# Performance work log

Hardware: AMD Instinct MI355X
Metric: run time of the kernel (lower is better)

The kernel has to match this reference:

```python
import jax, jax.numpy as jnp
import numpy as np
import math

EMB = 2048
N_Q = 32
N_KV = 8
HEAD = EMB // N_Q  # 64
N_REP = N_Q // N_KV  # 4
B, T = 2, 2048
ROPE_BASE = 10000.0


def setup_inputs() -> dict:
    key = jax.random.key(0)
    ks = jax.random.split(key, 9)
    s = 0.02
    return {
        "x": jax.random.normal(ks[0], (B, T, EMB), jnp.float32),
        "Wq": jax.random.normal(ks[1], (EMB, EMB), jnp.float32) * s,
        "bq": jax.random.normal(ks[2], (EMB,), jnp.float32) * s,
        "Wk": jax.random.normal(ks[3], (EMB, N_KV * HEAD), jnp.float32) * s,
        "bk": jax.random.normal(ks[4], (N_KV * HEAD,), jnp.float32) * s,
        "Wv": jax.random.normal(ks[5], (EMB, N_KV * HEAD), jnp.float32) * s,
        "bv": jax.random.normal(ks[6], (N_KV * HEAD,), jnp.float32) * s,
        "Wo": jax.random.normal(ks[7], (EMB, EMB), jnp.float32) * s,
        "bo": jax.random.normal(ks[8], (EMB,), jnp.float32) * s,
    }


def _rope_cos_sin(t, dim, dtype):
    inv_freq = 1.0 / (ROPE_BASE ** (jnp.arange(0, dim, 2, dtype=jnp.float32) / dim))
    freqs = jnp.arange(t, dtype=jnp.float32)[:, None] * inv_freq[None, :]  # (T, D/2)
    emb = jnp.concatenate([freqs, freqs], axis=-1)  # (T, D)
    return jnp.cos(emb).astype(dtype), jnp.sin(emb).astype(dtype)


def _rotate_half(x):
    d = x.shape[-1] // 2
    return jnp.concatenate([-x[..., d:], x[..., :d]], axis=-1)


def reference(x, Wq, bq, Wk, bk, Wv, bv, Wo, bo):
    b, t, c = x.shape
    q = (x @ Wq + bq).reshape(b, t, N_Q, HEAD)
    k = (x @ Wk + bk).reshape(b, t, N_KV, HEAD)
    v = (x @ Wv + bv).reshape(b, t, N_KV, HEAD)

    cos, sin = _rope_cos_sin(t, HEAD, x.dtype)  # (T, HEAD)
    cos = cos[None, :, None, :]
    sin = sin[None, :, None, :]
    q = q * cos + _rotate_half(q) * sin
    k = k * cos + _rotate_half(k) * sin

    # (B, H, T, D)
    q = q.transpose(0, 2, 1, 3)
    k = k.transpose(0, 2, 1, 3)
    v = v.transpose(0, 2, 1, 3)

    # repeat_kv: expand kv heads to match query heads
    k = jnp.repeat(k, N_REP, axis=1)
    v = jnp.repeat(v, N_REP, axis=1)

    scale = 1.0 / math.sqrt(HEAD)
    att = jnp.einsum("bhqd,bhkd->bhqk", q, k) * scale
    causal = jnp.tril(jnp.ones((t, t), dtype=bool))
    att = jnp.where(causal[None, None], att, jnp.finfo(att.dtype).min)
    att = jax.nn.softmax(att, axis=-1)

    y = jnp.einsum("bhqk,bhkd->bhqd", att, v)
    y = y.transpose(0, 2, 1, 3).reshape(b, t, c)
    return y @ Wo + bo
```

## Files before the change

kernel.cpp:

```cpp
#include <hip/hip_runtime.h>
#include <hip/hip_bf16.h>
#include <cstdint>
#include <cstddef>

typedef __attribute__((ext_vector_type(4))) float f32x4;
typedef __attribute__((ext_vector_type(8))) short bf16x8;

#define B_    2
#define T_    2048
#define EMB_  2048
#define NQ_   32
#define NKV_  8
#define HEAD_ 64
#define NTOT_ 3072
#define M_    (B_ * T_)
#define QBLK_ 128

__device__ __forceinline__ unsigned short f2bf(float f) {
  union { float f; unsigned int u; } v; v.f = f;
  unsigned int r = v.u + 0x7fffu + ((v.u >> 16) & 1u);
  return (unsigned short)(r >> 16);
}

__device__ __forceinline__ unsigned int pk_bf16(float lo, float hi) {
  __hip_bfloat162 h = __float22bfloat162_rn(make_float2(lo, hi));
  union { __hip_bfloat162 h; unsigned int u; } c; c.h = h;
  return c.u;
}

__device__ __forceinline__ void gload_lds16(const void* g, void* l) {
  __builtin_amdgcn_global_load_lds(
      (const __attribute__((address_space(1))) void*)g,
      (__attribute__((address_space(3))) void*)l, 16, 0, 0);
}


__global__ void cvt_bf16_kernel(const float* __restrict__ src,
                                unsigned short* __restrict__ dst, int n4) {
  int i = blockIdx.x * blockDim.x + threadIdx.x;
  if (i >= n4) return;
  float4 v = ((const float4*)src)[i];
  unsigned long long pk =
      (unsigned long long)f2bf(v.x) |
      ((unsigned long long)f2bf(v.y) << 16) |
      ((unsigned long long)f2bf(v.z) << 32) |
      ((unsigned long long)f2bf(v.w) << 48);
  *(unsigned long long*)(dst + (size_t)i * 4) = pk;
}

__global__ void transpose_cvt_kernel(const float* __restrict__ src,
                                     unsigned short* __restrict__ dst,
                                     int R, int C) {
  __shared__ float tile[32][33];
  int c0 = blockIdx.x * 32, r0 = blockIdx.y * 32;
  int tx = threadIdx.x, ty = threadIdx.y;
#pragma unroll
  for (int k = 0; k < 4; ++k)
    tile[ty + 8 * k][tx] = src[(size_t)(r0 + ty + 8 * k) * C + c0 + tx];
  __syncthreads();
#pragma unroll
  for (int k = 0; k < 4; ++k)
    dst[(size_t)(c0 + ty + 8 * k) * R + r0 + tx] = f2bf(tile[tx][ty + 8 * k]);
}

__global__ void concat_bias_kernel(const float* __restrict__ bq,
                                   const float* __restrict__ bk,
                                   const float* __restrict__ bv,
                                   float* __restrict__ dst) {
  int i = blockIdx.x * 256 + threadIdx.x;
  if (i < 2048) dst[i] = bq[i];
  else if (i < 2560) dst[i] = bk[i - 2048];
  else if (i < 3072) dst[i] = bv[i - 2560];
}

#define L2_10000 13.2877123795494f

__global__ void rope_q_kernel(const float* __restrict__ qkv,
                              unsigned short* __restrict__ Qh) {
  int idx = blockIdx.x * 256 + threadIdx.x;
  int i  = idx & 31;
  int h  = (idx >> 5) & 31;
  int bt = idx >> 10;
  int t  = bt & (T_ - 1);
  int b  = bt >> 11;
  float invf = exp2f(-(float)i * (L2_10000 / 32.f));
  float ang = (float)t * invf;
  float s, c; sincosf(ang, &s, &c);
  const float* row = qkv + (size_t)bt * NTOT_ + h * 64;
  float x1 = row[i], x2 = row[i + 32];
  unsigned short* q = Qh + ((size_t)(b * NQ_ + h) * T_ + t) * HEAD_;
  q[i]      = f2bf((x1 * c - x2 * s) * 0.125f);
  q[i + 32] = f2bf((x2 * c + x1 * s) * 0.125f);
}

__global__ void rope_k_kernel(const float* __restrict__ qkv,
                              unsigned short* __restrict__ Kh) {
  int idx = blockIdx.x * 256 + threadIdx.x;
  int i  = idx & 31;
  int kh = (idx >> 5) & 7;
  int bt = idx >> 8;
  int t  = bt & (T_ - 1);
  int b  = bt >> 11;
  float invf = exp2f(-(float)i * (L2_10000 / 32.f));
  float ang = (float)t * invf;
  float s, c; sincosf(ang, &s, &c);
  const float* row = qkv + (size_t)bt * NTOT_ + 2048 + kh * 64;
  float x1 = row[i], x2 = row[i + 32];
  unsigned short* kp = Kh + ((size_t)(b * NKV_ + kh) * T_ + t) * HEAD_;
  kp[i]      = f2bf(x1 * c - x2 * s);
  kp[i + 32] = f2bf(x2 * c + x1 * s);
}

__global__ void vt_kernel(const float* __restrict__ qkv,
                          unsigned short* __restrict__ Vt) {
  int idx = blockIdx.x * 256 + threadIdx.x;
  int t  = idx & (T_ - 1);
  int d  = (idx >> 11) & 63;
  int kh = (idx >> 17) & 7;
  int b  = idx >> 20;
  float v = qkv[(size_t)(b * T_ + t) * NTOT_ + 2560 + kh * 64 + d];
  Vt[((size_t)((b * NKV_ + kh) * 64 + d)) * T_ + t] = f2bf(v);
}


__launch_bounds__(256, 2)
__global__ void gemm_bt_bias(const unsigned short* __restrict__ A,
                             const unsigned short* __restrict__ BT,
                             const float* __restrict__ bias,
                             float* __restrict__ C, int N, int K) {
  __shared__ unsigned short Alds[128 * 32];
  __shared__ unsigned short Blds[128 * 32];
  const int tid = threadIdx.x;
  const int wave = tid >> 6, lane = tid & 63;
  const int l16 = lane & 15, lg = lane >> 4;
  const int m0 = blockIdx.x * 128;
  const int n0 = blockIdx.y * 128;
  const int wr = wave >> 1, wc = wave & 1;

  f32x4 zero4 = {0.f, 0.f, 0.f, 0.f};
  f32x4 acc[4][4];
#pragma unroll
  for (int i = 0; i < 4; ++i)
#pragma unroll
    for (int j = 0; j < 4; ++j) acc[i][j] = zero4;

  const int arow = tid >> 2;
  const int kcb  = (tid & 3) * 8;
  const int nk = K >> 5;
  for (int kt = 0; kt < nk; ++kt) {
    const int k0 = kt << 5;
    gload_lds16(A + (size_t)(m0 + arow) * K + k0 + kcb,       (char*)Alds + tid * 16);
    gload_lds16(A + (size_t)(m0 + 64 + arow) * K + k0 + kcb,  (char*)Alds + 4096 + tid * 16);
    gload_lds16(BT + (size_t)(n0 + arow) * K + k0 + kcb,      (char*)Blds + tid * 16);
    gload_lds16(BT + (size_t)(n0 + 64 + arow) * K + k0 + kcb, (char*)Blds + 4096 + tid * 16);
    __syncthreads();
    bf16x8 af[4], bfr[4];
#pragma unroll
    for (int i = 0; i < 4; ++i)
      af[i] = *(const bf16x8*)(Alds + (wr * 64 + i * 16 + l16) * 32 + lg * 8);
#pragma unroll
    for (int j = 0; j < 4; ++j)
      bfr[j] = *(const bf16x8*)(Blds + (wc * 64 + j * 16 + l16) * 32 + lg * 8);
#pragma unroll
    for (int i = 0; i < 4; ++i)
#pragma unroll
      for (int j = 0; j < 4; ++j)
        acc[i][j] = __builtin_amdgcn_mfma_f32_16x16x32_bf16(af[i], bfr[j], acc[i][j], 0, 0, 0);
    __syncthreads();
  }
#pragma unroll
  for (int j = 0; j < 4; ++j) {
    const int col = n0 + wc * 64 + j * 16 + l16;
    const float bv = bias[col];
#pragma unroll
    for (int i = 0; i < 4; ++i) {
      const int rowb = m0 + wr * 64 + i * 16 + lg * 4;
#pragma unroll
      for (int r = 0; r < 4; ++r)
        C[(size_t)(rowb + r) * N + col] = acc[i][j][r] + bv;
    }
  }
}


__launch_bounds__(256, 2)
__global__ void flash_attn_kernel(const unsigned short* __restrict__ Qh,
                                  const unsigned short* __restrict__ Kh,
                                  const unsigned short* __restrict__ Vt,
                                  unsigned short* __restrict__ Y) {
  __shared__ unsigned short Klds[2][64 * 64];
  __shared__ unsigned short Vlds[2][64 * 64];
  __shared__ unsigned short Plds[4][32 * 64];
  const int tid = threadIdx.x;
  const int wave = tid >> 6, lane = tid & 63;
  const int l16 = lane & 15, lg = lane >> 4;
  const int h = blockIdx.y, b = blockIdx.z;
  const int kh = h >> 2;

  const size_t kbase = (size_t)(b * NKV_ + kh) * T_ * HEAD_;
  const size_t vbase = (size_t)(b * NKV_ + kh) * HEAD_ * T_;
  const int srow = tid >> 3;
  const int csrc = (tid & 7) ^ (srow & 7);
  unsigned short* pl = Plds[wave];
  const f32x4 zero4 = {0.f, 0.f, 0.f, 0.f};

#define STAGE(bi, kv0) do {                                                         \
    gload_lds16(Kh + kbase + (size_t)((kv0) + srow) * HEAD_ + csrc * 8,             \
                (char*)Klds[bi] + tid * 16);                                        \
    gload_lds16(Kh + kbase + (size_t)((kv0) + srow + 32) * HEAD_ + csrc * 8,        \
                (char*)Klds[bi] + 4096 + tid * 16);                                 \
    gload_lds16(Vt + vbase + (size_t)srow * T_ + (kv0) + csrc * 8,                  \
                (char*)Vlds[bi] + tid * 16);                                        \
    gload_lds16(Vt + vbase + (size_t)(srow + 32) * T_ + (kv0) + csrc * 8,           \
                (char*)Vlds[bi] + 4096 + tid * 16);                                 \
  } while (0)

  for (int seg = 0; seg < 2; ++seg) {
    const int qt = seg ? (15 - (int)blockIdx.x) : (int)blockIdx.x;
    const int q0 = qt * QBLK_;
    const int nt = (q0 >> 6) + 2;

    bf16x8 aq[2][2];
#pragma unroll
    for (int qh = 0; qh < 2; ++qh) {
      const unsigned short* qp =
          Qh + ((size_t)(b * NQ_ + h) * T_ + q0 + wave * 32 + qh * 16 + l16) * HEAD_;
      aq[qh][0] = *(const bf16x8*)(qp + lg * 8);
      aq[qh][1] = *(const bf16x8*)(qp + 32 + lg * 8);
    }

    f32x4 oacc[2][4];
#pragma unroll
    for (int qh = 0; qh < 2; ++qh)
#pragma unroll
      for (int df = 0; df < 4; ++df) oacc[qh][df] = zero4;
    float mreg[2] = {-1e30f, -1e30f};
    float lp[2] = {0.f, 0.f};

    STAGE(0, 0);

    for (int t = 0; t < nt; ++t) {
      if (t + 1 < nt) {
        STAGE((t + 1) & 1, (t + 1) * 64);
        asm volatile("s_waitcnt vmcnt(4)" ::: "memory");
      } else {
        asm volatile("s_waitcnt vmcnt(0)" ::: "memory");
      }
      __builtin_amdgcn_s_barrier();
      __builtin_amdgcn_sched_barrier(0);

      const unsigned short* Kb = Klds[t & 1];
      const unsigned short* Vb = Vlds[t & 1];
      const int kv0 = t * 64;

      float p[2][4][4];
#pragma unroll
      for (int cf = 0; cf < 4; ++cf) {
        const int krow = cf * 16 + l16;
        const bf16x8 k0 = *(const bf16x8*)(Kb + krow * 64 + ((lg ^ (krow & 7)) << 3));
        const bf16x8 k1 = *(const bf16x8*)(Kb + krow * 64 + (((4 + lg) ^ (krow & 7)) << 3));
#pragma unroll
        for (int qh = 0; qh < 2; ++qh) {
          f32x4 z = zero4;
          z = __builtin_amdgcn_mfma_f32_16x16x32_bf16(k0, aq[qh][0], z, 0, 0, 0);
          z = __builtin_amdgcn_mfma_f32_16x16x32_bf16(k1, aq[qh][1], z, 0, 0, 0);
#pragma unroll
          for (int r = 0; r < 4; ++r) p[qh][cf][r] = z[r];
        }
      }

      if (t >= nt - 2) {
#pragma unroll
        for (int qh = 0; qh < 2; ++qh) {
          const int qg = q0 + wave * 32 + qh * 16 + l16;
#pragma unroll
          for (int cf = 0; cf < 4; ++cf)
#pragma unroll
            for (int r = 0; r < 4; ++r)
              if (kv0 + cf * 16 + lg * 4 + r > qg) p[qh][cf][r] = -1e30f;
        }
      }

#pragma unroll
      for (int qh = 0; qh < 2; ++qh) {
        float pm = p[qh][0][0];
#pragma unroll
        for (int cf = 0; cf < 4; ++cf)
#pragma unroll
          for (int r = 0; r < 4; ++r) pm = fmaxf(pm, p[qh][cf][r]);
        pm = fmaxf(pm, __shfl_xor(pm, 16, 64));
        pm = fmaxf(pm, __shfl_xor(pm, 32, 64));
        const float mnew = fmaxf(mreg[qh], pm);
        const float corr = __expf(mreg[qh] - mnew);
        mreg[qh] = mnew;
        lp[qh] *= corr;
#pragma unroll
        for (int df = 0; df < 4; ++df)
#pragma unroll
          for (int r = 0; r < 4; ++r) oacc[qh][df][r] *= corr;
        float ps = 0.f;
#pragma unroll
        for (int cf = 0; cf < 4; ++cf)
#pragma unroll
          for (int r = 0; r < 4; ++r) {
            const float e = __expf(p[qh][cf][r] - mnew);
            p[qh][cf][r] = e;
            ps += e;
          }
        lp[qh] += ps;
      }

#pragma unroll
      for (int qh = 0; qh < 2; ++qh) {
        const int row = qh * 16 + l16;
#pragma unroll
        for (int cf = 0; cf < 4; ++cf) {
          const unsigned int w0 = pk_bf16(p[qh][cf][0], p[qh][cf][1]);
          const unsigned int w1 = pk_bf16(p[qh][cf][2], p[qh][cf][3]);
          const int u = cf * 2 + (lg >> 1);
          char* ad = (char*)pl + row * 128 + ((u ^ (row & 7)) << 4) + ((lg & 1) << 3);
          *(unsigned long long*)ad =
              (unsigned long long)w0 | ((unsigned long long)w1 << 32);
        }
      }
      bf16x8 pf[2][2];
#pragma unroll
      for (int qh = 0; qh < 2; ++qh) {
        const int row = qh * 16 + l16;
#pragma unroll
        for (int k2 = 0; k2 < 2; ++k2) {
          const int u = k2 * 4 + lg;
          pf[qh][k2] = *(const bf16x8*)((char*)pl + row * 128 + ((u ^ (row & 7)) << 4));
        }
      }

#pragma unroll
      for (int df = 0; df < 4; ++df) {
        const int vrow = df * 16 + l16;
        const bf16x8 v0 = *(const bf16x8*)(Vb + vrow * 64 + ((lg ^ (vrow & 7)) << 3));
        const bf16x8 v1 = *(const bf16x8*)(Vb + vrow * 64 + (((4 + lg) ^ (vrow & 7)) << 3));
#pragma unroll
        for (int qh = 0; qh < 2; ++qh) {
          oacc[qh][df] = __builtin_amdgcn_mfma_f32_16x16x32_bf16(v0, pf[qh][0], oacc[qh][df], 0, 0, 0);
          oacc[qh][df] = __builtin_amdgcn_mfma_f32_16x16x32_bf16(v1, pf[qh][1], oacc[qh][df], 0, 0, 0);
        }
      }

      asm volatile("s_waitcnt lgkmcnt(0)" ::: "memory");
      __builtin_amdgcn_sched_barrier(0);
      __builtin_amdgcn_s_barrier();
    }

#pragma unroll
    for (int qh = 0; qh < 2; ++qh) {
      float lt = lp[qh];
      lt += __shfl_xor(lt, 16, 64);
      lt += __shfl_xor(lt, 32, 64);
      const float inv = 1.f / lt;
      const int tq = q0 + wave * 32 + qh * 16 + l16;
      unsigned short* yp = Y + ((size_t)(b * T_ + tq)) * EMB_ + h * HEAD_;
#pragma unroll
      for (int df = 0; df < 4; ++df) {
        const unsigned int w0 = pk_bf16(oacc[qh][df][0] * inv, oacc[qh][df][1] * inv);
        const unsigned int w1 = pk_bf16(oacc[qh][df][2] * inv, oacc[qh][df][3] * inv);
        *(unsigned long long*)(yp + df * 16 + lg * 4) =
            (unsigned long long)w0 | ((unsigned long long)w1 << 32);
      }
    }
  }
#undef STAGE
}


extern "C" void kernel_launch(void* const* d_in, const int* in_sizes, int n_in,
                              void* d_out, int out_size, void* d_ws, size_t ws_size,
                              hipStream_t stream) {
  const float* x  = (const float*)d_in[0];
  const float* Wq = (const float*)d_in[1];
  const float* bq = (const float*)d_in[2];
  const float* Wk = (const float*)d_in[3];
  const float* bk = (const float*)d_in[4];
  const float* Wv = (const float*)d_in[5];
  const float* bv = (const float*)d_in[6];
  const float* Wo = (const float*)d_in[7];
  const float* bo = (const float*)d_in[8];
  float* out = (float*)d_out;

  char* ws = (char*)d_ws;
  size_t off = 0;
  auto alloc = [&](size_t bytes) {
    void* p = ws + off;
    off += (bytes + 255) & ~(size_t)255;
    return p;
  };
  unsigned short* xb     = (unsigned short*)alloc((size_t)M_ * EMB_ * 2);
  unsigned short* WqkvT  = (unsigned short*)alloc((size_t)NTOT_ * EMB_ * 2);
  unsigned short* WoT    = (unsigned short*)alloc((size_t)EMB_ * EMB_ * 2);
  float*          bcat   = (float*)alloc((size_t)NTOT_ * 4);
  float*          QKVlin = (float*)alloc((size_t)M_ * NTOT_ * 4);
  unsigned short* Qh     = (unsigned short*)alloc((size_t)B_ * NQ_ * T_ * HEAD_ * 2);
  unsigned short* Kh     = (unsigned short*)alloc((size_t)B_ * NKV_ * T_ * HEAD_ * 2);
  unsigned short* Vt     = (unsigned short*)alloc((size_t)B_ * NKV_ * HEAD_ * T_ * 2);
  unsigned short* Yb     = (unsigned short*)alloc((size_t)M_ * EMB_ * 2);

  cvt_bf16_kernel<<<(M_ * EMB_ / 4 + 255) / 256, 256, 0, stream>>>(x, xb, M_ * EMB_ / 4);

  dim3 tb(32, 8);
  transpose_cvt_kernel<<<dim3(EMB_ / 32, EMB_ / 32), tb, 0, stream>>>(Wq, WqkvT, EMB_, EMB_);
  transpose_cvt_kernel<<<dim3(512 / 32, EMB_ / 32), tb, 0, stream>>>(Wk, WqkvT + (size_t)2048 * 2048, EMB_, 512);
  transpose_cvt_kernel<<<dim3(512 / 32, EMB_ / 32), tb, 0, stream>>>(Wv, WqkvT + (size_t)2560 * 2048, EMB_, 512);
  transpose_cvt_kernel<<<dim3(EMB_ / 32, EMB_ / 32), tb, 0, stream>>>(Wo, WoT, EMB_, EMB_);
  concat_bias_kernel<<<(NTOT_ + 255) / 256, 256, 0, stream>>>(bq, bk, bv, bcat);

  gemm_bt_bias<<<dim3(M_ / 128, NTOT_ / 128), 256, 0, stream>>>(xb, WqkvT, bcat, QKVlin, NTOT_, EMB_);

  rope_q_kernel<<<(B_ * T_ * NQ_ * 32) / 256, 256, 0, stream>>>(QKVlin, Qh);
  rope_k_kernel<<<(B_ * T_ * NKV_ * 32) / 256, 256, 0, stream>>>(QKVlin, Kh);
  vt_kernel<<<(B_ * NKV_ * HEAD_ * T_) / 256, 256, 0, stream>>>(QKVlin, Vt);

  flash_attn_kernel<<<dim3(8, NQ_, B_), 256, 0, stream>>>(Qh, Kh, Vt, Yb);

  gemm_bt_bias<<<dim3(M_ / 128, EMB_ / 128), 256, 0, stream>>>(Yb, WoT, bo, out, EMB_, EMB_);

  (void)in_sizes; (void)n_in; (void)out_size; (void)ws_size;
}
```

Measured before the change: 237.7 us.

## Emit bf16 QKV, use exp2 softmax with lazy rescale and MFMA row sums

The QKV projection now writes bf16 instead of fp32, which halves the intermediate traffic read by the rope and V-transpose kernels. The attention softmax folds log2(e) into the Q scale so it can use the raw v_exp_f32 instruction. It skips the running-max rescale unless the max grows by more than 8. Row sums are computed with an extra MFMA against a vector of ones rather than VALU adds and shuffles. This trades some precision (bf16 intermediate, bf16-rounded P in the denominator) for less memory traffic and less VALU work.

New measurement: 231.5 us. 2.6% less time.

```diff
diff --git a/kernel.cpp b/kernel.cpp
--- a/kernel.cpp
+++ b/kernel.cpp
@@ -16,16 +16,28 @@
 #define M_    (B_ * T_)
 #define QBLK_ 128
 
+#define MFMA_ __builtin_amdgcn_mfma_f32_16x16x32_bf16
+
 __device__ __forceinline__ unsigned short f2bf(float f) {
   union { float f; unsigned int u; } v; v.f = f;
   unsigned int r = v.u + 0x7fffu + ((v.u >> 16) & 1u);
   return (unsigned short)(r >> 16);
 }
 
+__device__ __forceinline__ float bf2f(unsigned short u) {
+  union { unsigned int u; float f; } v; v.u = (unsigned int)u << 16; return v.f;
+}
+
 __device__ __forceinline__ unsigned int pk_bf16(float lo, float hi) {
   __hip_bfloat162 h = __float22bfloat162_rn(make_float2(lo, hi));
   union { __hip_bfloat162 h; unsigned int u; } c; c.h = h;
   return c.u;
+}
+
+__device__ __forceinline__ float ex2(float x) {
+  float r;
+  asm("v_exp_f32 %0, %1" : "=v"(r) : "v"(x));
+  return r;
 }
 
 __device__ __forceinline__ void gload_lds16(const void* g, void* l) {
@@ -74,8 +86,9 @@
 }
 
 #define L2_10000 13.2877123795494f
-
-__global__ void rope_q_kernel(const float* __restrict__ qkv,
+#define QSCALE_  0.18033688011112043f
+
+__global__ void rope_q_kernel(const unsigned short* __restrict__ qkv,
                               unsigned short* __restrict__ Qh) {
   int idx = blockIdx.x * 256 + threadIdx.x;
   int i  = idx & 31;
@@ -86,14 +99,14 @@
   float invf = exp2f(-(float)i * (L2_10000 / 32.f));
   float ang = (float)t * invf;
   float s, c; sincosf(ang, &s, &c);
-  const float* row = qkv + (size_t)bt * NTOT_ + h * 64;
-  float x1 = row[i], x2 = row[i + 32];
+  const unsigned short* row = qkv + (size_t)bt * NTOT_ + h * 64;
+  float x1 = bf2f(row[i]), x2 = bf2f(row[i + 32]);
   unsigned short* q = Qh + ((size_t)(b * NQ_ + h) * T_ + t) * HEAD_;
-  q[i]      = f2bf((x1 * c - x2 * s) * 0.125f);
-  q[i + 32] = f2bf((x2 * c + x1 * s) * 0.125f);
-}
-
-__global__ void rope_k_kernel(const float* __restrict__ qkv,
+  q[i]      = f2bf((x1 * c - x2 * s) * QSCALE_);
+  q[i + 32] = f2bf((x2 * c + x1 * s) * QSCALE_);
+}
+
+__global__ void rope_k_kernel(const unsigned short* __restrict__ qkv,
                               unsigned short* __restrict__ Kh) {
   int idx = blockIdx.x * 256 + threadIdx.x;
   int i  = idx & 31;
@@ -104,30 +117,31 @@
   float invf = exp2f(-(float)i * (L2_10000 / 32.f));
   float ang = (float)t * invf;
   float s, c; sincosf(ang, &s, &c);
-  const float* row = qkv + (size_t)bt * NTOT_ + 2048 + kh * 64;
-  float x1 = row[i], x2 = row[i + 32];
+  const unsigned short* row = qkv + (size_t)bt * NTOT_ + 2048 + kh * 64;
+  float x1 = bf2f(row[i]), x2 = bf2f(row[i + 32]);
   unsigned short* kp = Kh + ((size_t)(b * NKV_ + kh) * T_ + t) * HEAD_;
   kp[i]      = f2bf(x1 * c - x2 * s);
   kp[i + 32] = f2bf(x2 * c + x1 * s);
 }
 
-__global__ void vt_kernel(const float* __restrict__ qkv,
+__global__ void vt_kernel(const unsigned short* __restrict__ qkv,
                           unsigned short* __restrict__ Vt) {
   int idx = blockIdx.x * 256 + threadIdx.x;
   int t  = idx & (T_ - 1);
   int d  = (idx >> 11) & 63;
   int kh = (idx >> 17) & 7;
   int b  = idx >> 20;
-  float v = qkv[(size_t)(b * T_ + t) * NTOT_ + 2560 + kh * 64 + d];
-  Vt[((size_t)((b * NKV_ + kh) * 64 + d)) * T_ + t] = f2bf(v);
-}
-
-
+  Vt[((size_t)((b * NKV_ + kh) * 64 + d)) * T_ + t] =
+      qkv[(size_t)(b * T_ + t) * NTOT_ + 2560 + kh * 64 + d];
+}
+
+
+template <typename OutT>
 __launch_bounds__(256, 2)
 __global__ void gemm_bt_bias(const unsigned short* __restrict__ A,
                              const unsigned short* __restrict__ BT,
                              const float* __restrict__ bias,
-                             float* __restrict__ C, int N, int K) {
+                             OutT* __restrict__ C, int N, int K) {
   __shared__ unsigned short Alds[128 * 32];
   __shared__ unsigned short Blds[128 * 32];
   const int tid = threadIdx.x;
@@ -165,7 +179,7 @@
     for (int i = 0; i < 4; ++i)
 #pragma unroll
       for (int j = 0; j < 4; ++j)
-        acc[i][j] = __builtin_amdgcn_mfma_f32_16x16x32_bf16(af[i], bfr[j], acc[i][j], 0, 0, 0);
+        acc[i][j] = MFMA_(af[i], bfr[j], acc[i][j], 0, 0, 0);
     __syncthreads();
   }
 #pragma unroll
@@ -176,8 +190,13 @@
     for (int i = 0; i < 4; ++i) {
       const int rowb = m0 + wr * 64 + i * 16 + lg * 4;
 #pragma unroll
-      for (int r = 0; r < 4; ++r)
-        C[(size_t)(rowb + r) * N + col] = acc[i][j][r] + bv;
+      for (int r = 0; r < 4; ++r) {
+        const float v = acc[i][j][r] + bv;
+        if constexpr (sizeof(OutT) == 2)
+          C[(size_t)(rowb + r) * N + col] = (OutT)f2bf(v);
+        else
+          C[(size_t)(rowb + r) * N + col] = (OutT)v;
+      }
     }
   }
 }
@@ -203,6 +222,9 @@
   const int csrc = (tid & 7) ^ (srow & 7);
   unsigned short* pl = Plds[wave];
   const f32x4 zero4 = {0.f, 0.f, 0.f, 0.f};
+  const short one_bf = (short)0x3F80;
+  const bf16x8 onesv = {one_bf, one_bf, one_bf, one_bf,
+                        one_bf, one_bf, one_bf, one_bf};
 
 #define STAGE(bi, kv0) do {                                                         \
     gload_lds16(Kh + kbase + (size_t)((kv0) + srow) * HEAD_ + csrc * 8,             \
@@ -230,12 +252,14 @@
     }
 
     f32x4 oacc[2][4];
-#pragma unroll
-    for (int qh = 0; qh < 2; ++qh)
+    f32x4 lsum[2];
+#pragma unroll
+    for (int qh = 0; qh < 2; ++qh) {
+      lsum[qh] = zero4;
 #pragma unroll
       for (int df = 0; df < 4; ++df) oacc[qh][df] = zero4;
+    }
     float mreg[2] = {-1e30f, -1e30f};
-    float lp[2] = {0.f, 0.f};
 
     STAGE(0, 0);
 
@@ -262,8 +286,8 @@
 #pragma unroll
         for (int qh = 0; qh < 2; ++qh) {
           f32x4 z = zero4;
-          z = __builtin_amdgcn_mfma_f32_16x16x32_bf16(k0, aq[qh][0], z, 0, 0, 0);
-          z = __builtin_amdgcn_mfma_f32_16x16x32_bf16(k1, aq[qh][1], z, 0, 0, 0);
+          z = MFMA_(k0, aq[qh][0], z, 0, 0, 0);
+          z = MFMA_(k1, aq[qh][1], z, 0, 0, 0);
 #pragma unroll
           for (int r = 0; r < 4; ++r) p[qh][cf][r] = z[r];
         }
@@ -281,34 +305,41 @@
         }
       }
 
+      float mn[2];
 #pragma unroll
       for (int qh = 0; qh < 2; ++qh) {
-        float pm = p[qh][0][0];
+        float m = mreg[qh];
+#pragma unroll
+        for (int cf = 0; cf < 4; ++cf) {
+          m = fmaxf(m, fmaxf(p[qh][cf][0], p[qh][cf][1]));
+          m = fmaxf(m, fmaxf(p[qh][cf][2], p[qh][cf][3]));
+        }
+        m = fmaxf(m, __shfl_xor(m, 16, 64));
+        m = fmaxf(m, __shfl_xor(m, 32, 64));
+        mn[qh] = m;
+      }
+
+      const float dmax = fmaxf(mn[0] - mreg[0], mn[1] - mreg[1]);
+      if (!__all(dmax <= 8.f)) {
+#pragma unroll
+        for (int qh = 0; qh < 2; ++qh) {
+          const float corr = ex2(mreg[qh] - mn[qh]);
+          mreg[qh] = mn[qh];
+          lsum[qh][0] *= corr;
+#pragma unroll
+          for (int df = 0; df < 4; ++df)
+#pragma unroll
+            for (int r = 0; r < 4; ++r) oacc[qh][df][r] *= corr;
+        }
+      }
+
+#pragma unroll
+      for (int qh = 0; qh < 2; ++qh)
 #pragma unroll
         for (int cf = 0; cf < 4; ++cf)
 #pragma unroll
-          for (int r = 0; r < 4; ++r) pm = fmaxf(pm, p[qh][cf][r]);
-        pm = fmaxf(pm, __shfl_xor(pm, 16, 64));
-        pm = fmaxf(pm, __shfl_xor(pm, 32, 64));
-        const float mnew = fmaxf(mreg[qh], pm);
-        const float corr = __expf(mreg[qh] - mnew);
-        mreg[qh] = mnew;
-        lp[qh] *= corr;
-#pragma unroll
-        for (int df = 0; df < 4; ++df)
-#pragma unroll
-          for (int r = 0; r < 4; ++r) oacc[qh][df][r] *= corr;
-        float ps = 0.f;
-#pragma unroll
-        for (int cf = 0; cf < 4; ++cf)
-#pragma unroll
-          for (int r = 0; r < 4; ++r) {
-            const float e = __expf(p[qh][cf][r] - mnew);
-            p[qh][cf][r] = e;
-            ps += e;
-          }
-        lp[qh] += ps;
-      }
+          for (int r = 0; r < 4; ++r)
+            p[qh][cf][r] = ex2(p[qh][cf][r] - mreg[qh]);
 
 #pragma unroll
       for (int qh = 0; qh < 2; ++qh) {
@@ -335,14 +366,19 @@
       }
 
 #pragma unroll
+      for (int qh = 0; qh < 2; ++qh) {
+        lsum[qh] = MFMA_(onesv, pf[qh][0], lsum[qh], 0, 0, 0);
+        lsum[qh] = MFMA_(onesv, pf[qh][1], lsum[qh], 0, 0, 0);
+      }
+#pragma unroll
       for (int df = 0; df < 4; ++df) {
         const int vrow = df * 16 + l16;
         const bf16x8 v0 = *(const bf16x8*)(Vb + vrow * 64 + ((lg ^ (vrow & 7)) << 3));
         const bf16x8 v1 = *(const bf16x8*)(Vb + vrow * 64 + (((4 + lg) ^ (vrow & 7)) << 3));
 #pragma unroll
         for (int qh = 0; qh < 2; ++qh) {
-          oacc[qh][df] = __builtin_amdgcn_mfma_f32_16x16x32_bf16(v0, pf[qh][0], oacc[qh][df], 0, 0, 0);
-          oacc[qh][df] = __builtin_amdgcn_mfma_f32_16x16x32_bf16(v1, pf[qh][1], oacc[qh][df], 0, 0, 0);
+          oacc[qh][df] = MFMA_(v0, pf[qh][0], oacc[qh][df], 0, 0, 0);
+          oacc[qh][df] = MFMA_(v1, pf[qh][1], oacc[qh][df], 0, 0, 0);
         }
       }
 
@@ -353,10 +389,7 @@
 
 #pragma unroll
     for (int qh = 0; qh < 2; ++qh) {
-      float lt = lp[qh];
-      lt += __shfl_xor(lt, 16, 64);
-      lt += __shfl_xor(lt, 32, 64);
-      const float inv = 1.f / lt;
+      const float inv = 1.f / lsum[qh][0];
       const int tq = q0 + wave * 32 + qh * 16 + l16;
       unsigned short* yp = Y + ((size_t)(b * T_ + tq)) * EMB_ + h * HEAD_;
 #pragma unroll
@@ -397,7 +430,7 @@
   unsigned short* WqkvT  = (unsigned short*)alloc((size_t)NTOT_ * EMB_ * 2);
   unsigned short* WoT    = (unsigned short*)alloc((size_t)EMB_ * EMB_ * 2);
   float*          bcat   = (float*)alloc((size_t)NTOT_ * 4);
-  float*          QKVlin = (float*)alloc((size_t)M_ * NTOT_ * 4);
+  unsigned short* QKVlin = (unsigned short*)alloc((size_t)M_ * NTOT_ * 2);
   unsigned short* Qh     = (unsigned short*)alloc((size_t)B_ * NQ_ * T_ * HEAD_ * 2);
   unsigned short* Kh     = (unsigned short*)alloc((size_t)B_ * NKV_ * T_ * HEAD_ * 2);
   unsigned short* Vt     = (unsigned short*)alloc((size_t)B_ * NKV_ * HEAD_ * T_ * 2);
@@ -412,7 +445,8 @@
   transpose_cvt_kernel<<<dim3(EMB_ / 32, EMB_ / 32), tb, 0, stream>>>(Wo, WoT, EMB_, EMB_);
   concat_bias_kernel<<<(NTOT_ + 255) / 256, 256, 0, stream>>>(bq, bk, bv, bcat);
 
-  gemm_bt_bias<<<dim3(M_ / 128, NTOT_ / 128), 256, 0, stream>>>(xb, WqkvT, bcat, QKVlin, NTOT_, EMB_);
+  gemm_bt_bias<unsigned short><<<dim3(M_ / 128, NTOT_ / 128), 256, 0, stream>>>(
+      xb, WqkvT, bcat, QKVlin, NTOT_, EMB_);
 
   rope_q_kernel<<<(B_ * T_ * NQ_ * 32) / 256, 256, 0, stream>>>(QKVlin, Qh);
   rope_k_kernel<<<(B_ * T_ * NKV_ * 32) / 256, 256, 0, stream>>>(QKVlin, Kh);
@@ -420,7 +454,8 @@
 
   flash_attn_kernel<<<dim3(8, NQ_, B_), 256, 0, stream>>>(Qh, Kh, Vt, Yb);
 
-  gemm_bt_bias<<<dim3(M_ / 128, EMB_ / 128), 256, 0, stream>>>(Yb, WoT, bo, out, EMB_, EMB_);
+  gemm_bt_bias<float><<<dim3(M_ / 128, EMB_ / 128), 256, 0, stream>>>(
+      Yb, WoT, bo, out, EMB_, EMB_);
 
   (void)in_sizes; (void)n_in; (void)out_size; (void)ws_size;
 }
```
